# Optimization experiments

Measured on AMD Instinct MI355X. Metric: run time of the kernel, lower is better.

## Reference

```python
import jax, jax.numpy as jnp
import numpy as np

B, T, D, H = 2, 2048, 1024, 16
DH = D // H  # 64


def setup_inputs() -> dict:
    key = jax.random.key(0)
    ks = jax.random.split(key, 8)
    s = 0.02  # typical init scale for projection weights
    return {
        "query_states": jax.random.normal(ks[0], (B, T, D), jnp.float32),
        "key_states": jax.random.normal(ks[1], (B, T, D), jnp.float32),
        "attention_mask": jnp.zeros((B, 1, 1, T), jnp.float32),
        "Wq": jax.random.normal(ks[2], (D, D), jnp.float32) * s,
        "bq": jnp.zeros((D,), jnp.float32),
        "Wk": jax.random.normal(ks[3], (D, D), jnp.float32) * s,
        "bk": jnp.zeros((D,), jnp.float32),
        "Wv": jax.random.normal(ks[4], (D, D), jnp.float32) * s,
        "bv": jnp.zeros((D,), jnp.float32),
        "mask_future": 0,
    }


def _heads(x):
    # [B, T, D] -> [B, H, T, DH]
    b, t, _ = x.shape
    return x.reshape(b, t, H, DH).transpose(0, 2, 1, 3)


def reference(query_states, key_states, attention_mask, Wq, bq, Wk, bk, Wv, bv, mask_future):
    q = _heads(query_states @ Wq + bq)   # [B,H,T,DH]
    k = _heads(key_states @ Wk + bk)     # [B,H,T,DH]
    v = _heads(key_states @ Wv + bv)     # [B,H,T,DH]
    scale = 1.0 / jnp.sqrt(jnp.asarray(DH, jnp.float32))
    scores = jnp.einsum("bhqd,bhkd->bhqk", q, k) * scale + attention_mask
    if mask_future:  # static Python int flag
        t = scores.shape[-1]
        triu = jnp.triu(jnp.ones((t, t), bool))  # includes diagonal, as in torch.triu
        scores = jnp.where(triu, -jnp.inf, scores)
    probs = jax.nn.softmax(scores, axis=-1)
    # dropout p=0.0 -> identity
    ctx = jnp.einsum("bhqk,bhkd->bhqd", probs, v)  # [B,H,T,DH]
    b, _, t, _ = ctx.shape
    return ctx.transpose(0, 2, 1, 3).reshape(b, t, H * DH)
```

## Files before the change

kernel.cpp:

```cpp
#include <hip/hip_runtime.h>

#define DEV __device__ __forceinline__

typedef _Float16 f16;
typedef __attribute__((ext_vector_type(2))) _Float16 f16x2;
typedef __attribute__((ext_vector_type(8))) _Float16 f16x8;
typedef __attribute__((ext_vector_type(4))) float f32x4;
typedef __attribute__((ext_vector_type(16))) float f32x16;

constexpr int B = 2, T = 2048, D = 1024, H = 16, DH = 64;
constexpr int M = B * T;
constexpr float LOG2E = 1.4426950408889634f;

DEV void gload_lds16(const void* g, void* l) {
  __builtin_amdgcn_global_load_lds(
      (const __attribute__((address_space(1))) void*)g,
      (__attribute__((address_space(3))) void*)l, 16, 0, 0);
}

DEV unsigned pack_pk(float a, float b) {
  auto v = __builtin_amdgcn_cvt_pkrtz(a, b);
  return __builtin_bit_cast(unsigned, v);
}

__global__ __launch_bounds__(256) void cast_f32_f16(
    const float* __restrict__ in, f16* __restrict__ out, int n) {
  int i = (blockIdx.x * 256 + threadIdx.x) * 8;
  if (i >= n) return;
  f32x4 a = *(const f32x4*)(in + i);
  f32x4 b = *(const f32x4*)(in + i + 4);
  f16x8 o;
  o[0] = (f16)a[0]; o[1] = (f16)a[1]; o[2] = (f16)a[2]; o[3] = (f16)a[3];
  o[4] = (f16)b[0]; o[5] = (f16)b[1]; o[6] = (f16)b[2]; o[7] = (f16)b[3];
  *(f16x8*)(out + i) = o;
}

__global__ __launch_bounds__(256) void transpose_cast(
    const float* __restrict__ Wq, const float* __restrict__ Wk,
    const float* __restrict__ Wv, f16* __restrict__ WT) {
  int mat = blockIdx.z;
  const float* W = (mat == 0) ? Wq : (mat == 1 ? Wk : Wv);
  f16* out = WT + (size_t)mat * D * D;
  __shared__ float tile[32][33];
  int nt = blockIdx.x * 32, kt = blockIdx.y * 32;
  int tx = threadIdx.x, ty = threadIdx.y;
  for (int j = 0; j < 4; ++j) {
    int r = ty + 8 * j;
    tile[r][tx] = W[(size_t)(kt + r) * D + nt + tx];
  }
  __syncthreads();
  for (int j = 0; j < 4; ++j) {
    int r = ty + 8 * j;
    out[(size_t)(nt + r) * D + kt + tx] = (f16)tile[tx][r];
  }
}

__global__ __launch_bounds__(256) void qkv_gemm(
    const f16* __restrict__ XQ, const f16* __restrict__ XK,
    const f16* __restrict__ WT, const float* __restrict__ bq,
    const float* __restrict__ bk, const float* __restrict__ bv,
    f16* __restrict__ QKV) {
  int mat = blockIdx.z;
  const f16* X = (mat == 0) ? XQ : XK;
  const f16* Wt = WT + (size_t)mat * D * D;
  const float* bias = (mat == 0) ? bq : (mat == 1 ? bk : bv);
  f16* out = QKV + (size_t)mat * M * D;
  float oscale = (mat == 0) ? 0.125f * LOG2E : 1.0f;
  int m0 = blockIdx.y * 128, n0 = blockIdx.x * 128;

  __shared__ f16 lA[128 * 64];
  __shared__ f16 lB[128 * 64];
  char* lAb = (char*)lA;
  char* lBb = (char*)lB;

  int tid = threadIdx.x;
  int w = tid >> 6, lane = tid & 63;
  int l15 = lane & 15, lhi = lane >> 4;
  int wr = w >> 1, wc = w & 1;
  int r8 = lane >> 3, slot = lane & 7;
  int sslot = slot ^ r8;

  f32x4 acc[4][4] = {};

  for (int kt = 0; kt < D / 64; ++kt) {
    __syncthreads();
    for (int i = 0; i < 4; ++i) {
      int chunk = w * 4 + i;
      int row = chunk * 8 + r8;
      const f16* srcA = X + (size_t)(m0 + row) * D + kt * 64 + sslot * 8;
      gload_lds16(srcA, lAb + chunk * 1024);
      const f16* srcB = Wt + (size_t)(n0 + row) * D + kt * 64 + sslot * 8;
      gload_lds16(srcB, lBb + chunk * 1024);
    }
    __syncthreads();
    for (int ks = 0; ks < 2; ++ks) {
      f16x8 aF[4], bF[4];
      for (int mt = 0; mt < 4; ++mt) {
        int row = wr * 64 + mt * 16 + l15;
        int byt = row * 128 + ks * 64 + lhi * 16;
        byt ^= (row & 7) << 4;
        aF[mt] = *(const f16x8*)(lAb + byt);
      }
      for (int nt = 0; nt < 4; ++nt) {
        int row = wc * 64 + nt * 16 + l15;
        int byt = row * 128 + ks * 64 + lhi * 16;
        byt ^= (row & 7) << 4;
        bF[nt] = *(const f16x8*)(lBb + byt);
      }
      for (int mt = 0; mt < 4; ++mt)
        for (int nt = 0; nt < 4; ++nt)
          acc[mt][nt] = __builtin_amdgcn_mfma_f32_16x16x32_f16(
              aF[mt], bF[nt], acc[mt][nt], 0, 0, 0);
    }
  }

  float bv4[4];
  for (int nt = 0; nt < 4; ++nt) bv4[nt] = bias[n0 + wc * 64 + nt * 16 + l15];
  for (int mt = 0; mt < 4; ++mt)
    for (int nt = 0; nt < 4; ++nt) {
      int col = n0 + wc * 64 + nt * 16 + l15;
      for (int r = 0; r < 4; ++r) {
        int row = m0 + wr * 64 + mt * 16 + lhi * 4 + r;
        out[(size_t)row * D + col] = (f16)((acc[mt][nt][r] + bv4[nt]) * oscale);
      }
    }
}

__global__ __launch_bounds__(256) void transpose_v(
    const f16* __restrict__ QKV, f16* __restrict__ VT) {
  const f16* V = QKV + (size_t)2 * M * D;
  int b = blockIdx.z, h = blockIdx.y, t0 = blockIdx.x * 64;
  __shared__ unsigned tl[64 * 32];
  char* tb = (char*)tl;
  int tid = threadIdx.x;
  int rp = tid >> 3, d0 = (tid & 7) * 8;
  const f16* src = V + (size_t)(b * T + t0 + 2 * rp) * D + h * 64 + d0;
  f16x8 a = *(const f16x8*)(src);
  f16x8 c = *(const f16x8*)(src + D);
#pragma unroll
  for (int j = 0; j < 8; ++j) {
    int d = d0 + j;
    f16x2 pr; pr[0] = a[j]; pr[1] = c[j];
    unsigned pk = __builtin_bit_cast(unsigned, pr);
    int byt = (d * 128 + rp * 4) ^ (((d >> 3) & 3) << 5);
    *(unsigned*)(tb + byt) = pk;
  }
  __syncthreads();
  int d = tid >> 2, c2 = tid & 3;
  int rbase = (d * 128 + c2 * 32) ^ (((d >> 3) & 3) << 5);
  uint4 x = *(uint4*)(tb + rbase);
  uint4 y = *(uint4*)(tb + rbase + 16);
  f16* dst = VT + ((size_t)(b * H + h) * 64 + d) * T + t0 + c2 * 16;
  *(uint4*)(dst) = x;
  *(uint4*)(dst + 8) = y;
}

__global__ __launch_bounds__(256, 2) void attn(
    const f16* __restrict__ QKV, const f16* __restrict__ VT,
    const float* __restrict__ mask, const int* __restrict__ mfp,
    float* __restrict__ out) {
  const f16* Q = QKV;
  const f16* K = QKV + (size_t)M * D;
  int b = blockIdx.z, h = blockIdx.y, q0 = blockIdx.x * 128;
  int mf = *mfp;
  constexpr int NT = T / 64;

  __shared__ f16 sK[2][64 * 64];
  __shared__ f16 sVT[2][64 * 64];
  __shared__ f16 sP[4][32 * 64];
  __shared__ float sMask[T];
  __shared__ int sMnz;

  int tid = threadIdx.x;
  int w = tid >> 6, lane = tid & 63;
  int l31 = lane & 31, hi = lane >> 5, l7 = lane & 7;
  int qrow = q0 + w * 32 + l31;
  char* sPw = (char*)sP[w];

  if (tid == 0) sMnz = 0;
  const float* mb = mask + (size_t)b * T;
  bool lnz = false;
#pragma unroll
  for (int i = 0; i < 2; ++i) {
    int idx = (tid + i * 256) * 4;
    f32x4 mv = *(const f32x4*)(mb + idx);
    f32x4 ms;
#pragma unroll
    for (int j = 0; j < 4; ++j) {
      ms[j] = mv[j] * LOG2E;
      lnz |= (mv[j] != 0.f);
    }
    *(f32x4*)(sMask + idx) = ms;
  }

  f16x8 qF[4];
  const f16* qp = Q + (size_t)(b * T + qrow) * D + h * 64;
#pragma unroll
  for (int kc = 0; kc < 4; ++kc) qF[kc] = *(const f16x8*)(qp + kc * 16 + hi * 8);

  auto STAGE = [&](int kv0, int buf) {
    char* dK = (char*)sK[buf];
    char* dV = (char*)sVT[buf];
#pragma unroll
    for (int i = 0; i < 2; ++i) {
      int c = (w * 2 + i) * 64 + lane;
      int r = c >> 3;
      int slot = (c & 7) ^ (r & 7);
      const f16* srcK = K + (size_t)(b * T + kv0 + r) * D + h * 64 + slot * 8;
      gload_lds16(srcK, dK + (w * 2 + i) * 1024);
      const f16* srcV = VT + ((size_t)(b * H + h) * 64 + r) * T + kv0 + slot * 8;
      gload_lds16(srcV, dV + (w * 2 + i) * 1024);
    }
  };

  float mprev = -1e30f, lsum = 0.f;
  f32x16 oAcc[2] = {};

  __syncthreads();
  if (lnz) sMnz = 1;
  STAGE(0, 0);
  __syncthreads();
  int domask = sMnz | mf;

  for (int t = 0; t < NT; ++t) {
    if (t) __syncthreads();
    if (t + 1 < NT) STAGE((t + 1) * 64, (t + 1) & 1);
    int kv0 = t * 64;
    char* bK = (char*)sK[t & 1];
    char* bV = (char*)sVT[t & 1];

    f32x16 sA[2] = {};
#pragma unroll
    for (int f = 0; f < 2; ++f) {
#pragma unroll
      for (int kc = 0; kc < 4; ++kc) {
        int row = f * 32 + l31;
        f16x8 kF = *(const f16x8*)(bK + ((row * 128 + kc * 32 + hi * 16) ^ (l7 << 4)));
        sA[f] = __builtin_amdgcn_mfma_f32_32x32x16_f16(kF, qF[kc], sA[f], 0, 0, 0);
      }
    }

    float mx = -1e30f;
    if (domask) {
#pragma unroll
      for (int f = 0; f < 2; ++f)
#pragma unroll
        for (int r = 0; r < 16; ++r) {
          int kv = kv0 + f * 32 + (r & 3) + 8 * (r >> 2) + 4 * hi;
          float v = sA[f][r] + sMask[kv];
          if (mf && kv >= qrow) v = -1e30f;
          sA[f][r] = v;
          mx = fmaxf(mx, v);
        }
    } else {
#pragma unroll
      for (int f = 0; f < 2; ++f)
#pragma unroll
        for (int r = 0; r < 16; ++r) mx = fmaxf(mx, sA[f][r]);
    }
    mx = fmaxf(mx, __shfl_xor(mx, 32, 64));

    if (!__all(mx <= mprev + 8.f)) {
      float mn = fmaxf(mprev, mx);
      float asc = __builtin_amdgcn_exp2f(mprev - mn);
      lsum *= asc;
#pragma unroll
      for (int f = 0; f < 2; ++f)
#pragma unroll
        for (int r = 0; r < 16; ++r) oAcc[f][r] *= asc;
      mprev = mn;
    }

    float rs = 0.f;
#pragma unroll
    for (int f = 0; f < 2; ++f)
#pragma unroll
      for (int r = 0; r < 16; ++r) {
        float e = __builtin_amdgcn_exp2f(sA[f][r] - mprev);
        sA[f][r] = e;
        rs += e;
      }
    rs += __shfl_xor(rs, 32, 64);
    lsum += rs;

#pragma unroll
    for (int f = 0; f < 2; ++f)
#pragma unroll
      for (int g = 0; g < 4; ++g) {
        int byt = (l31 * 128 + f * 64 + g * 16 + hi * 8) ^ (l7 << 4);
        uint2 u;
        u.x = pack_pk(sA[f][g * 4 + 0], sA[f][g * 4 + 1]);
        u.y = pack_pk(sA[f][g * 4 + 2], sA[f][g * 4 + 3]);
        *(uint2*)(sPw + byt) = u;
      }

    f16x8 pF[4];
#pragma unroll
    for (int kc = 0; kc < 4; ++kc)
      pF[kc] = *(const f16x8*)(sPw + ((l31 * 128 + kc * 32 + hi * 16) ^ (l7 << 4)));
#pragma unroll
    for (int df = 0; df < 2; ++df)
#pragma unroll
      for (int kc = 0; kc < 4; ++kc) {
        int row = df * 32 + l31;
        f16x8 vF = *(const f16x8*)(bV + ((row * 128 + kc * 32 + hi * 16) ^ (l7 << 4)));
        oAcc[df] = __builtin_amdgcn_mfma_f32_32x32x16_f16(vF, pF[kc], oAcc[df], 0, 0, 0);
      }
  }

  float linv = 1.0f / lsum;
  float* op = out + (size_t)(b * T + qrow) * D + h * 64;
#pragma unroll
  for (int df = 0; df < 2; ++df)
#pragma unroll
    for (int g = 0; g < 4; ++g) {
      f32x4 ov;
#pragma unroll
      for (int r2 = 0; r2 < 4; ++r2) ov[r2] = oAcc[df][g * 4 + r2] * linv;
      *(f32x4*)(op + df * 32 + g * 8 + hi * 4) = ov;
    }
}

extern "C" void kernel_launch(void* const* d_in, const int* in_sizes, int n_in,
                              void* d_out, int out_size, void* d_ws, size_t ws_size,
                              hipStream_t stream) {
  const float* q_in = (const float*)d_in[0];
  const float* k_in = (const float*)d_in[1];
  const float* amask = (const float*)d_in[2];
  const float* Wq = (const float*)d_in[3];
  const float* bq = (const float*)d_in[4];
  const float* Wk = (const float*)d_in[5];
  const float* bk = (const float*)d_in[6];
  const float* Wv = (const float*)d_in[7];
  const float* bv = (const float*)d_in[8];
  const int* mf = (const int*)d_in[9];
  float* out = (float*)d_out;

  char* ws = (char*)d_ws;
  f16* XQ = (f16*)ws;
  f16* XK = (f16*)(ws + (((size_t)8) << 20));
  f16* WT = (f16*)(ws + (((size_t)16) << 20));
  f16* QKV = (f16*)(ws + (((size_t)24) << 20));
  f16* VT = (f16*)(ws + (((size_t)48) << 20));

  cast_f32_f16<<<2048, 256, 0, stream>>>(q_in, XQ, M * D);
  cast_f32_f16<<<2048, 256, 0, stream>>>(k_in, XK, M * D);
  transpose_cast<<<dim3(32, 32, 3), dim3(32, 8), 0, stream>>>(Wq, Wk, Wv, WT);
  qkv_gemm<<<dim3(8, 32, 3), 256, 0, stream>>>(XQ, XK, WT, bq, bk, bv, QKV);
  transpose_v<<<dim3(32, 16, 2), 256, 0, stream>>>(QKV, VT);
  attn<<<dim3(16, 16, 2), 256, 0, stream>>>(QKV, VT, amask, mf, out);
}
```

Measured before the change: 213.1 us.

## Write head-major Q/K and transposed V from GEMM, drop transpose kernel, shuffle P in registers

The QKV GEMM epilogue now writes Q and K in [B,H,T,64] layout and V directly transposed as [B,H,64,T]. This removes the separate transpose_v kernel and gives attention contiguous per-head tiles. Inside attention, P is repacked into MFMA operands with cross-lane shuffles instead of an LDS round trip, and the shared mask buffer is dropped in favour of a wave-level any-nonzero check with direct global mask reads. The launch bounds hint is relaxed and blocks are remapped so heads are grouped together. The trade-off is scattered, less-coalesced epilogue stores in the GEMM.

```diff
diff --git a/kernel.cpp b/kernel.cpp
--- a/kernel.cpp
+++ b/kernel.cpp
@@ -4,9 +4,11 @@
 
 typedef _Float16 f16;
 typedef __attribute__((ext_vector_type(2))) _Float16 f16x2;
+typedef __attribute__((ext_vector_type(4))) _Float16 f16x4;
 typedef __attribute__((ext_vector_type(8))) _Float16 f16x8;
 typedef __attribute__((ext_vector_type(4))) float f32x4;
 typedef __attribute__((ext_vector_type(16))) float f32x16;
+typedef __attribute__((ext_vector_type(4))) int i32x4;
 
 constexpr int B = 2, T = 2048, D = 1024, H = 16, DH = 64;
 constexpr int M = B * T;
@@ -22,6 +24,9 @@
   auto v = __builtin_amdgcn_cvt_pkrtz(a, b);
   return __builtin_bit_cast(unsigned, v);
 }
+
+DEV float redmax32(float x) { return fmaxf(x, __shfl_xor(x, 32, 64)); }
+DEV float redsum32(float x) { return x + __shfl_xor(x, 32, 64); }
 
 __global__ __launch_bounds__(256) void cast_f32_f16(
     const float* __restrict__ in, f16* __restrict__ out, int n) {
@@ -66,7 +71,8 @@
   const float* bias = (mat == 0) ? bq : (mat == 1 ? bk : bv);
   f16* out = QKV + (size_t)mat * M * D;
   float oscale = (mat == 0) ? 0.125f * LOG2E : 1.0f;
-  int m0 = blockIdx.y * 128, n0 = blockIdx.x * 128;
+  int Lb = blockIdx.x + 8 * blockIdx.y;
+  int n0 = (Lb & 7) * 128, m0 = (Lb >> 3) * 128;
 
   __shared__ f16 lA[128 * 64];
   __shared__ f16 lB[128 * 64];
@@ -97,14 +103,12 @@
       f16x8 aF[4], bF[4];
       for (int mt = 0; mt < 4; ++mt) {
         int row = wr * 64 + mt * 16 + l15;
-        int byt = row * 128 + ks * 64 + lhi * 16;
-        byt ^= (row & 7) << 4;
+        int byt = (row * 128 + ks * 64 + lhi * 16) ^ ((row & 7) << 4);
         aF[mt] = *(const f16x8*)(lAb + byt);
       }
       for (int nt = 0; nt < 4; ++nt) {
         int row = wc * 64 + nt * 16 + l15;
-        int byt = row * 128 + ks * 64 + lhi * 16;
-        byt ^= (row & 7) << 4;
+        int byt = (row * 128 + ks * 64 + lhi * 16) ^ ((row & 7) << 4);
         bF[nt] = *(const f16x8*)(lBb + byt);
       }
       for (int mt = 0; mt < 4; ++mt)
@@ -116,85 +120,66 @@
 
   float bv4[4];
   for (int nt = 0; nt < 4; ++nt) bv4[nt] = bias[n0 + wc * 64 + nt * 16 + l15];
-  for (int mt = 0; mt < 4; ++mt)
-    for (int nt = 0; nt < 4; ++nt) {
-      int col = n0 + wc * 64 + nt * 16 + l15;
-      for (int r = 0; r < 4; ++r) {
-        int row = m0 + wr * 64 + mt * 16 + lhi * 4 + r;
-        out[(size_t)row * D + col] = (f16)((acc[mt][nt][r] + bv4[nt]) * oscale);
-      }
-    }
-}
-
-__global__ __launch_bounds__(256) void transpose_v(
-    const f16* __restrict__ QKV, f16* __restrict__ VT) {
-  const f16* V = QKV + (size_t)2 * M * D;
-  int b = blockIdx.z, h = blockIdx.y, t0 = blockIdx.x * 64;
-  __shared__ unsigned tl[64 * 32];
-  char* tb = (char*)tl;
-  int tid = threadIdx.x;
-  int rp = tid >> 3, d0 = (tid & 7) * 8;
-  const f16* src = V + (size_t)(b * T + t0 + 2 * rp) * D + h * 64 + d0;
-  f16x8 a = *(const f16x8*)(src);
-  f16x8 c = *(const f16x8*)(src + D);
-#pragma unroll
-  for (int j = 0; j < 8; ++j) {
-    int d = d0 + j;
-    f16x2 pr; pr[0] = a[j]; pr[1] = c[j];
-    unsigned pk = __builtin_bit_cast(unsigned, pr);
-    int byt = (d * 128 + rp * 4) ^ (((d >> 3) & 3) << 5);
-    *(unsigned*)(tb + byt) = pk;
-  }
-  __syncthreads();
-  int d = tid >> 2, c2 = tid & 3;
-  int rbase = (d * 128 + c2 * 32) ^ (((d >> 3) & 3) << 5);
-  uint4 x = *(uint4*)(tb + rbase);
-  uint4 y = *(uint4*)(tb + rbase + 16);
-  f16* dst = VT + ((size_t)(b * H + h) * 64 + d) * T + t0 + c2 * 16;
-  *(uint4*)(dst) = x;
-  *(uint4*)(dst + 8) = y;
-}
-
-__global__ __launch_bounds__(256, 2) void attn(
-    const f16* __restrict__ QKV, const f16* __restrict__ VT,
-    const float* __restrict__ mask, const int* __restrict__ mfp,
-    float* __restrict__ out) {
-  const f16* Q = QKV;
-  const f16* K = QKV + (size_t)M * D;
-  int b = blockIdx.z, h = blockIdx.y, q0 = blockIdx.x * 128;
+  if (mat < 2) {
+    for (int mt = 0; mt < 4; ++mt)
+      for (int nt = 0; nt < 4; ++nt) {
+        int col = n0 + wc * 64 + nt * 16 + l15;
+        int hh = col >> 6, dh = col & 63;
+        for (int r = 0; r < 4; ++r) {
+          int row = m0 + wr * 64 + mt * 16 + lhi * 4 + r;
+          int bb = row >> 11, tt = row & (T - 1);
+          out[((size_t)(bb * H + hh) * T + tt) * 64 + dh] =
+              (f16)((acc[mt][nt][r] + bv4[nt]) * oscale);
+        }
+      }
+  } else {
+    for (int mt = 0; mt < 4; ++mt)
+      for (int nt = 0; nt < 4; ++nt) {
+        int col = n0 + wc * 64 + nt * 16 + l15;
+        int hh = col >> 6, dh = col & 63;
+        int row0 = m0 + wr * 64 + mt * 16 + lhi * 4;
+        int bb = row0 >> 11, tt = row0 & (T - 1);
+        f16x4 pk;
+        for (int r = 0; r < 4; ++r) pk[r] = (f16)(acc[mt][nt][r] + bv4[nt]);
+        *(f16x4*)(out + ((size_t)(bb * H + hh) * 64 + dh) * T + tt) = pk;
+      }
+  }
+}
+
+__global__ __launch_bounds__(256) void attn(
+    const f16* __restrict__ QKV, const float* __restrict__ mask,
+    const int* __restrict__ mfp, float* __restrict__ out) {
+  int L = blockIdx.x + 16 * blockIdx.y + 256 * blockIdx.z;
+  int e = L & 7, q = L >> 3;
+  int bh = e * 4 + (q & 3);
+  int q0 = (q >> 2) * 128;
+  int b = bh >> 4, h = bh & 15;
   int mf = *mfp;
   constexpr int NT = T / 64;
 
+  const f16* Qh = QKV + (size_t)bh * T * 64;
+  const f16* Kh = QKV + (size_t)M * D + (size_t)bh * T * 64;
+  const f16* VTh = QKV + (size_t)2 * M * D + (size_t)bh * 64 * T;
+
   __shared__ f16 sK[2][64 * 64];
   __shared__ f16 sVT[2][64 * 64];
-  __shared__ f16 sP[4][32 * 64];
-  __shared__ float sMask[T];
-  __shared__ int sMnz;
 
   int tid = threadIdx.x;
   int w = tid >> 6, lane = tid & 63;
-  int l31 = lane & 31, hi = lane >> 5, l7 = lane & 7;
+  int l31 = lane & 31, hi = lane >> 5;
   int qrow = q0 + w * 32 + l31;
-  char* sPw = (char*)sP[w];
-
-  if (tid == 0) sMnz = 0;
+
   const float* mb = mask + (size_t)b * T;
   bool lnz = false;
 #pragma unroll
-  for (int i = 0; i < 2; ++i) {
-    int idx = (tid + i * 256) * 4;
-    f32x4 mv = *(const f32x4*)(mb + idx);
-    f32x4 ms;
-#pragma unroll
-    for (int j = 0; j < 4; ++j) {
-      ms[j] = mv[j] * LOG2E;
-      lnz |= (mv[j] != 0.f);
-    }
-    *(f32x4*)(sMask + idx) = ms;
-  }
+  for (int j = 0; j < 8; ++j) {
+    f32x4 mv = *(const f32x4*)(mb + lane * 32 + j * 4);
+    lnz |= (mv[0] != 0.f) | (mv[1] != 0.f) | (mv[2] != 0.f) | (mv[3] != 0.f);
+  }
+  int domask = __any(lnz) | mf;
 
   f16x8 qF[4];
-  const f16* qp = Q + (size_t)(b * T + qrow) * D + h * 64;
+  const f16* qp = Qh + (size_t)qrow * 64;
 #pragma unroll
   for (int kc = 0; kc < 4; ++kc) qF[kc] = *(const f16x8*)(qp + kc * 16 + hi * 8);
 
@@ -206,39 +191,32 @@
       int c = (w * 2 + i) * 64 + lane;
       int r = c >> 3;
       int slot = (c & 7) ^ (r & 7);
-      const f16* srcK = K + (size_t)(b * T + kv0 + r) * D + h * 64 + slot * 8;
-      gload_lds16(srcK, dK + (w * 2 + i) * 1024);
-      const f16* srcV = VT + ((size_t)(b * H + h) * 64 + r) * T + kv0 + slot * 8;
-      gload_lds16(srcV, dV + (w * 2 + i) * 1024);
+      gload_lds16(Kh + (size_t)(kv0 + r) * 64 + slot * 8, dK + (w * 2 + i) * 1024);
+      gload_lds16(VTh + (size_t)r * T + kv0 + slot * 8, dV + (w * 2 + i) * 1024);
     }
   };
 
   float mprev = -1e30f, lsum = 0.f;
   f32x16 oAcc[2] = {};
-
-  __syncthreads();
-  if (lnz) sMnz = 1;
   STAGE(0, 0);
   __syncthreads();
-  int domask = sMnz | mf;
 
   for (int t = 0; t < NT; ++t) {
     if (t) __syncthreads();
     if (t + 1 < NT) STAGE((t + 1) * 64, (t + 1) & 1);
     int kv0 = t * 64;
-    char* bK = (char*)sK[t & 1];
-    char* bV = (char*)sVT[t & 1];
+    const char* bK = (const char*)sK[t & 1];
+    const char* bV = (const char*)sVT[t & 1];
 
     f32x16 sA[2] = {};
 #pragma unroll
-    for (int f = 0; f < 2; ++f) {
+    for (int f = 0; f < 2; ++f)
 #pragma unroll
       for (int kc = 0; kc < 4; ++kc) {
         int row = f * 32 + l31;
-        f16x8 kF = *(const f16x8*)(bK + ((row * 128 + kc * 32 + hi * 16) ^ (l7 << 4)));
+        f16x8 kF = *(const f16x8*)(bK + ((row * 128 + kc * 32 + hi * 16) ^ ((row & 7) << 4)));
         sA[f] = __builtin_amdgcn_mfma_f32_32x32x16_f16(kF, qF[kc], sA[f], 0, 0, 0);
       }
-    }
 
     float mx = -1e30f;
     if (domask) {
@@ -247,7 +225,7 @@
 #pragma unroll
         for (int r = 0; r < 16; ++r) {
           int kv = kv0 + f * 32 + (r & 3) + 8 * (r >> 2) + 4 * hi;
-          float v = sA[f][r] + sMask[kv];
+          float v = sA[f][r] + LOG2E * mb[kv];
           if (mf && kv >= qrow) v = -1e30f;
           sA[f][r] = v;
           mx = fmaxf(mx, v);
@@ -258,7 +236,7 @@
 #pragma unroll
         for (int r = 0; r < 16; ++r) mx = fmaxf(mx, sA[f][r]);
     }
-    mx = fmaxf(mx, __shfl_xor(mx, 32, 64));
+    mx = redmax32(mx);
 
     if (!__all(mx <= mprev + 8.f)) {
       float mn = fmaxf(mprev, mx);
@@ -276,34 +254,39 @@
     for (int f = 0; f < 2; ++f)
 #pragma unroll
       for (int r = 0; r < 16; ++r) {
-        float e = __builtin_amdgcn_exp2f(sA[f][r] - mprev);
-        sA[f][r] = e;
-        rs += e;
-      }
-    rs += __shfl_xor(rs, 32, 64);
-    lsum += rs;
-
-#pragma unroll
-    for (int f = 0; f < 2; ++f)
-#pragma unroll
-      for (int g = 0; g < 4; ++g) {
-        int byt = (l31 * 128 + f * 64 + g * 16 + hi * 8) ^ (l7 << 4);
-        uint2 u;
-        u.x = pack_pk(sA[f][g * 4 + 0], sA[f][g * 4 + 1]);
-        u.y = pack_pk(sA[f][g * 4 + 2], sA[f][g * 4 + 3]);
-        *(uint2*)(sPw + byt) = u;
-      }
+        float e2 = __builtin_amdgcn_exp2f(sA[f][r] - mprev);
+        sA[f][r] = e2;
+        rs += e2;
+      }
+    lsum += redsum32(rs);
 
     f16x8 pF[4];
 #pragma unroll
-    for (int kc = 0; kc < 4; ++kc)
-      pF[kc] = *(const f16x8*)(sPw + ((l31 * 128 + kc * 32 + hi * 16) ^ (l7 << 4)));
+    for (int f = 0; f < 2; ++f) {
+      unsigned pk_[8], px_[8];
+#pragma unroll
+      for (int g = 0; g < 8; ++g) {
+        pk_[g] = pack_pk(sA[f][2 * g], sA[f][2 * g + 1]);
+        px_[g] = (unsigned)__shfl_xor((int)pk_[g], 32, 64);
+      }
+#pragma unroll
+      for (int half = 0; half < 2; ++half) {
+        int o = half * 4;
+        i32x4 d;
+        d[0] = (int)(hi ? px_[o + 2] : pk_[o + 0]);
+        d[1] = (int)(hi ? px_[o + 3] : pk_[o + 1]);
+        d[2] = (int)(hi ? pk_[o + 2] : px_[o + 0]);
+        d[3] = (int)(hi ? pk_[o + 3] : px_[o + 1]);
+        pF[f * 2 + half] = __builtin_bit_cast(f16x8, d);
+      }
+    }
+
 #pragma unroll
     for (int df = 0; df < 2; ++df)
 #pragma unroll
       for (int kc = 0; kc < 4; ++kc) {
         int row = df * 32 + l31;
-        f16x8 vF = *(const f16x8*)(bV + ((row * 128 + kc * 32 + hi * 16) ^ (l7 << 4)));
+        f16x8 vF = *(const f16x8*)(bV + ((row * 128 + kc * 32 + hi * 16) ^ ((row & 7) << 4)));
         oAcc[df] = __builtin_amdgcn_mfma_f32_32x32x16_f16(vF, pF[kc], oAcc[df], 0, 0, 0);
       }
   }
@@ -341,12 +324,10 @@
   f16* XK = (f16*)(ws + (((size_t)8) << 20));
   f16* WT = (f16*)(ws + (((size_t)16) << 20));
   f16* QKV = (f16*)(ws + (((size_t)24) << 20));
-  f16* VT = (f16*)(ws + (((size_t)48) << 20));
 
   cast_f32_f16<<<2048, 256, 0, stream>>>(q_in, XQ, M * D);
   cast_f32_f16<<<2048, 256, 0, stream>>>(k_in, XK, M * D);
   transpose_cast<<<dim3(32, 32, 3), dim3(32, 8), 0, stream>>>(Wq, Wk, Wv, WT);
   qkv_gemm<<<dim3(8, 32, 3), 256, 0, stream>>>(XQ, XK, WT, bq, bk, bv, QKV);
-  transpose_v<<<dim3(32, 16, 2), 256, 0, stream>>>(QKV, VT);
-  attn<<<dim3(16, 16, 2), 256, 0, stream>>>(QKV, VT, amask, mf, out);
-}
+  attn<<<dim3(16, 16, 2), 256, 0, stream>>>(QKV, amask, mf, out);
+}
```

After: 218.5 us. 2.5% more time.
